# Performance work log

Hardware: AMD Instinct MI355X
Metric: run time of the kernel (lower is better)

Reference implementation:

```python
import jax, jax.numpy as jnp
import numpy as np

E = 2048      # embed_dim
H = 16        # num_heads
HD = E // H // 2   # differential head dim = 64
S = 2048      # seq len
B = 1         # batch
DEPTH = 12
LAMBDA_INIT = 0.8 - 0.6 * float(np.exp(-0.3 * DEPTH))
EPS = 1e-5


def setup_inputs() -> dict:
    key = jax.random.key(0)
    ks = jax.random.split(key, 12)
    n = lambda k, shape, s=1.0: (jax.random.normal(k, shape, dtype=jnp.float32) * s)
    return {
        "query": n(ks[0], (S, B, E)),
        "key": n(ks[1], (S, B, E)),
        "value": n(ks[2], (S, B, E)),
        "rel_pos": 0,
        "attn_mask": jnp.zeros((B, S), dtype=jnp.bool_),
        "Wq": n(ks[3], (E, E), 0.02),
        "Wk": n(ks[4], (E, E), 0.02),
        "Wv": n(ks[5], (E, E), 0.02),
        "Wo": n(ks[6], (E, E), 0.02),
        "lq1": n(ks[7], (HD,), 0.1),
        "lk1": n(ks[8], (HD,), 0.1),
        "lq2": n(ks[9], (HD,), 0.1),
        "lk2": n(ks[10], (HD,), 0.1),
        "subln_g": jnp.ones((2 * HD,), dtype=jnp.float32),
    }


def reference(query, key, value, rel_pos, attn_mask,
              Wq, Wk, Wv, Wo, lq1, lk1, lq2, lk2, subln_g):
    # (S,B,E) -> (B,S,E)
    q = jnp.einsum("sbe,fe->bsf", query, Wq)
    k = jnp.einsum("sbe,fe->bsf", key, Wk)
    v = jnp.einsum("sbe,fe->bsf", value, Wv)

    bsz, tgt_len, _ = q.shape
    scaling = HD ** -0.5

    q = q.reshape(bsz, tgt_len, 2 * H, HD).transpose(0, 2, 1, 3) * scaling  # (B,2H,S,hd)
    k = k.reshape(bsz, tgt_len, 2 * H, HD).transpose(0, 2, 1, 3)            # (B,2H,S,hd)
    v = v.reshape(bsz, tgt_len, H, 2 * HD).transpose(0, 2, 1, 3)            # (B,H,S,2hd)

    scores = jnp.einsum("bhqd,bhkd->bhqk", q, k)  # (B,2H,S,S)
    mask = jnp.where(attn_mask[:, None, None, :], -jnp.inf, 0.0).astype(scores.dtype)
    scores = jnp.nan_to_num(scores + mask)  # torch.nan_to_num: nan->0, -inf->finite min

    probs = jax.nn.softmax(scores.astype(jnp.float32), axis=-1).astype(scores.dtype)
    probs = jnp.clip(probs, -1e6, 1e6)  # clamp as in original (dropout is identity in eval)

    lam1 = jnp.exp(jnp.sum(lq1 * lk1))
    lam2 = jnp.exp(jnp.sum(lq2 * lk2))
    lam_full = lam1 - lam2 + LAMBDA_INIT

    probs = probs.reshape(bsz, H, 2, tgt_len, tgt_len)
    diff = probs[:, :, 0] - lam_full * probs[:, :, 1]   # (B,H,S,S)

    attn = jnp.einsum("bhqk,bhkd->bhqd", diff, v)       # (B,H,S,2hd)

    # RMSNorm over last dim with affine weight
    rms = jax.lax.rsqrt(jnp.mean(jnp.square(attn), axis=-1, keepdims=True) + EPS)
    attn = attn * rms * subln_g
    attn = attn * (1.0 - LAMBDA_INIT)

    attn = attn.transpose(0, 2, 1, 3).reshape(bsz, tgt_len, H * 2 * HD)  # (B,S,E)
    attn = attn.transpose(1, 0, 2)                                       # (S,B,E)
    return jnp.einsum("sbe,fe->sbf", attn, Wo)
```

## Files before the change

### kernel.cpp

```cpp
#include <hip/hip_runtime.h>
#include <stdint.h>

#define LAMBDA_INIT_F 0.7836057665f

typedef __bf16 bf16x8 __attribute__((ext_vector_type(8)));
typedef float  f32x4  __attribute__((ext_vector_type(4)));
typedef unsigned short u16x8 __attribute__((ext_vector_type(8)));
typedef unsigned short u16x4 __attribute__((ext_vector_type(4)));
typedef short s16x4 __attribute__((ext_vector_type(4)));

__device__ __forceinline__ unsigned short f2b(float f) {
    union { float f; unsigned u; } v; v.f = f;
    unsigned u = v.u;
    return (unsigned short)((u + 0x7fffu + ((u >> 16) & 1u)) >> 16);
}

__device__ __forceinline__ unsigned pk2(float a, float b) {
    unsigned ua = __float_as_uint(a) + 0x8000u;
    unsigned ub = __float_as_uint(b) + 0x8000u;
    return __builtin_amdgcn_perm(ub, ua, 0x07060302u);
}

#if __has_builtin(__builtin_amdgcn_exp2f)
#define EXP2(x) __builtin_amdgcn_exp2f(x)
#else
__device__ __forceinline__ float EXP2(float x) {
    float r; asm volatile("v_exp_f32 %0, %1\n\ts_nop 1" : "=v"(r) : "v"(x)); return r;
}
#endif

#define GLD16(gp, sp) __builtin_amdgcn_global_load_lds( \
    (const __attribute__((address_space(1))) void*)(uintptr_t)(gp), \
    (__attribute__((address_space(3))) void*)(uint32_t)(uintptr_t)(sp), 16, 0, 0)

__global__ __launch_bounds__(256) void cvt7(const float* __restrict__ s0, const float* __restrict__ s1,
                                            const float* __restrict__ s2, const float* __restrict__ s3,
                                            const float* __restrict__ s4, const float* __restrict__ s5,
                                            const float* __restrict__ s6,
                                            unsigned short* __restrict__ dst) {
    int z = blockIdx.y;
    const float* s = z == 0 ? s0 : z == 1 ? s1 : z == 2 ? s2 : z == 3 ? s3 : z == 4 ? s4 : z == 5 ? s5 : s6;
    unsigned short* d = dst + (size_t)z * 4194304;
    size_t i = ((size_t)blockIdx.x * 256 + threadIdx.x) * 8;
    float4 a = *(const float4*)(s + i);
    float4 b = *(const float4*)(s + i + 4);
    u16x8 o;
    o[0] = f2b(a.x); o[1] = f2b(a.y); o[2] = f2b(a.z); o[3] = f2b(a.w);
    o[4] = f2b(b.x); o[5] = f2b(b.y); o[6] = f2b(b.z); o[7] = f2b(b.w);
    *(u16x8*)(d + i) = o;
}

template <int OUT_BF16, int NT, int DO_VT, int WPB>
__global__ __launch_bounds__(256, WPB) void gemm_bt(const unsigned short* __restrict__ Abase,
                                                    const unsigned short* __restrict__ Bbase,
                                                    void* __restrict__ Cbase,
                                                    unsigned short* __restrict__ VT,
                                                    float alpha0) {
    constexpr int MI = (NT == 128) ? 4 : 2;
    __shared__ __align__(16) unsigned short As[128 * 32];
    __shared__ __align__(16) unsigned short Bs[NT * 32];
    const int tid = threadIdx.x;
    const int w = tid >> 6, lane = tid & 63;
    const int quad = lane >> 4, l16 = lane & 15;
    const int b = blockIdx.z;
    const unsigned short* A = Abase + (size_t)b * 4194304;
    const unsigned short* B = Bbase + (size_t)b * 4194304;
    const float alpha = (b == 0) ? alpha0 : 1.0f;
    const int m0 = blockIdx.y * 128, n0 = blockIdx.x * NT;
    const int wm = (NT == 128) ? (w >> 1) * 64 : w * 32;
    const int wn = (NT == 128) ? (w & 1) * 64 : 0;
    const int sr = lane >> 2;
    const int sc = (((lane & 3) ^ ((lane >> 3) & 3)) * 8);
    const int rsw = ((l16 >> 1) & 3);

    f32x4 zz = {0.f, 0.f, 0.f, 0.f};
    f32x4 acc[MI][4];
#pragma unroll
    for (int i = 0; i < MI; ++i)
#pragma unroll
        for (int jn = 0; jn < 4; ++jn) acc[i][jn] = zz;

    for (int k0 = 0; k0 < 2048; k0 += 32) {
        GLD16(A + (size_t)(m0 + w * 16 + sr) * 2048 + k0 + sc,      &As[(w * 16) * 32]);
        GLD16(A + (size_t)(m0 + 64 + w * 16 + sr) * 2048 + k0 + sc, &As[(64 + w * 16) * 32]);
        if (NT == 128) {
            GLD16(B + (size_t)(n0 + w * 16 + sr) * 2048 + k0 + sc,      &Bs[(w * 16) * 32]);
            GLD16(B + (size_t)(n0 + 64 + w * 16 + sr) * 2048 + k0 + sc, &Bs[(64 + (w * 16)) * 32]);
        } else {
            GLD16(B + (size_t)(n0 + w * 16 + sr) * 2048 + k0 + sc, &Bs[(w * 16) * 32]);
        }
        __syncthreads();
        bf16x8 af[MI], bfr[4];
#pragma unroll
        for (int i = 0; i < MI; ++i) af[i]  = *(const bf16x8*)&As[(wm + i * 16 + l16) * 32 + (quad ^ rsw) * 8];
#pragma unroll
        for (int i = 0; i < 4; ++i)  bfr[i] = *(const bf16x8*)&Bs[(wn + i * 16 + l16) * 32 + (quad ^ rsw) * 8];
#pragma unroll
        for (int i = 0; i < MI; ++i)
#pragma unroll
            for (int jn = 0; jn < 4; ++jn)
                acc[i][jn] = __builtin_amdgcn_mfma_f32_16x16x32_bf16(af[i], bfr[jn], acc[i][jn], 0, 0, 0);
        __syncthreads();
    }

    if (DO_VT && b == 2) {
#pragma unroll
        for (int i = 0; i < MI; ++i)
#pragma unroll
            for (int jn = 0; jn < 4; ++jn) {
                int n = n0 + wn + jn * 16 + l16;
                int m = m0 + wm + i * 16 + quad * 4;
                u16x4 o;
#pragma unroll
                for (int r = 0; r < 4; ++r) o[r] = f2b(acc[i][jn][r]);
                *(u16x4*)&VT[(size_t)n * 2048 + m] = o;
            }
    } else {
#pragma unroll
        for (int i = 0; i < MI; ++i)
#pragma unroll
            for (int jn = 0; jn < 4; ++jn)
#pragma unroll
                for (int r = 0; r < 4; ++r) {
                    int row = m0 + wm + i * 16 + quad * 4 + r;
                    int col = n0 + wn + jn * 16 + l16;
                    float v = acc[i][jn][r] * alpha;
                    if (OUT_BF16)
                        ((unsigned short*)Cbase + (size_t)b * 4194304)[(size_t)row * 2048 + col] = f2b(v);
                    else
                        ((float*)Cbase)[(size_t)row * 2048 + col] = v;
                }
    }
}

__global__ __launch_bounds__(256, 2) void diff_attn(const unsigned short* __restrict__ qb,
                                                    const unsigned short* __restrict__ kb,
                                                    const unsigned short* __restrict__ vt,
                                                    const float* __restrict__ lq1,
                                                    const float* __restrict__ lk1,
                                                    const float* __restrict__ lq2,
                                                    const float* __restrict__ lk2,
                                                    const float* __restrict__ g,
                                                    unsigned short* __restrict__ Aout) {
    __shared__ __align__(16) unsigned short Ks[128 * 128];
    __shared__ __align__(16) unsigned short Vs[128 * 128];
    __shared__ float lam_s;
    const int tid = threadIdx.x, w = tid >> 6, lane = tid & 63;
    const int quad = lane >> 4, l16 = lane & 15;
    const int j = blockIdx.y;
    const int q0 = blockIdx.x * 64;

    if (tid < 64) {
        float p1 = lq1[tid] * lk1[tid];
        float p2 = lq2[tid] * lk2[tid];
        for (int off = 32; off; off >>= 1) { p1 += __shfl_xor(p1, off, 64); p2 += __shfl_xor(p2, off, 64); }
        if (tid == 0) lam_s = __expf(p1) - __expf(p2) + LAMBDA_INIT_F;
    }

    bf16x8 qf[2][2];
#pragma unroll
    for (int p = 0; p < 2; ++p)
#pragma unroll
        for (int dh = 0; dh < 2; ++dh)
            qf[p][dh] = *(const bf16x8*)&qb[(size_t)(q0 + w * 16 + l16) * 2048 + j * 128 + p * 64 + dh * 32 + quad * 8];

    f32x4 O[2][8];
#pragma unroll
    for (int p = 0; p < 2; ++p)
#pragma unroll
        for (int i = 0; i < 8; ++i)
#pragma unroll
            for (int r = 0; r < 4; ++r) O[p][i][r] = 0.f;
    float lsum[2] = {0.f, 0.f};

    const int srow = lane >> 4;

    for (int kv0 = 0; kv0 < 2048; kv0 += 128) {
#pragma unroll
        for (int t = 0; t < 8; ++t) {
            int rb = (w * 8 + t) * 4;
            int row = rb + srow;
            int cbs = (((lane & 15) ^ (row & 15)) * 8);
            GLD16(kb + (size_t)(kv0 + row) * 2048 + j * 128 + cbs, &Ks[rb * 128]);
            GLD16(vt + (size_t)(j * 128 + row) * 2048 + kv0 + cbs, &Vs[rb * 128]);
        }
        __syncthreads();

        s16x4 pf[2][8];
#pragma unroll
        for (int p = 0; p < 2; ++p) {
#pragma unroll
            for (int i = 0; i < 8; ++i) {
                bf16x8 a0 = *(const bf16x8*)&Ks[(i * 16 + l16) * 128 + ((p * 8 + quad) ^ l16) * 8];
                bf16x8 a1 = *(const bf16x8*)&Ks[(i * 16 + l16) * 128 + ((p * 8 + 4 + quad) ^ l16) * 8];
                f32x4 s = {0.f, 0.f, 0.f, 0.f};
                s = __builtin_amdgcn_mfma_f32_16x16x32_bf16(a0, qf[p][0], s, 0, 0, 0);
                s = __builtin_amdgcn_mfma_f32_16x16x32_bf16(a1, qf[p][1], s, 0, 0, 0);
                float e0 = EXP2(s[0]), e1 = EXP2(s[1]), e2 = EXP2(s[2]), e3 = EXP2(s[3]);
                lsum[p] += (e0 + e1) + (e2 + e3);
                unsigned d0 = pk2(e0, e1), d1 = pk2(e2, e3);
                s16x4 pv;
                pv[0] = (short)(d0 & 0xffff); pv[1] = (short)(d0 >> 16);
                pv[2] = (short)(d1 & 0xffff); pv[3] = (short)(d1 >> 16);
                pf[p][i] = pv;
            }
        }
#pragma unroll
        for (int i = 0; i < 8; ++i) {
#pragma unroll
            for (int dt = 0; dt < 8; ++dt) {
                int blk = (i * 2 + (quad >> 1)) ^ l16;
                s16x4 vf = *(const s16x4*)&Vs[(dt * 16 + l16) * 128 + blk * 8 + (quad & 1) * 4];
                O[0][dt] = __builtin_amdgcn_mfma_f32_16x16x16bf16_1k(vf, pf[0][i], O[0][dt], 0, 0, 0);
                O[1][dt] = __builtin_amdgcn_mfma_f32_16x16x16bf16_1k(vf, pf[1][i], O[1][dt], 0, 0, 0);
            }
        }
        __syncthreads();
    }

#pragma unroll
    for (int p = 0; p < 2; ++p) {
        lsum[p] += __shfl_xor(lsum[p], 16, 64);
        lsum[p] += __shfl_xor(lsum[p], 32, 64);
    }
    const float inv1 = 1.0f / lsum[0];
    const float inv2 = lam_s / lsum[1];

    float ssum = 0.f;
#pragma unroll
    for (int dt = 0; dt < 8; ++dt)
#pragma unroll
        for (int r = 0; r < 4; ++r) {
            float v = O[0][dt][r] * inv1 - O[1][dt][r] * inv2;
            O[0][dt][r] = v;
            ssum += v * v;
        }
    ssum += __shfl_xor(ssum, 16, 64);
    ssum += __shfl_xor(ssum, 32, 64);
    const float rms = rsqrtf(ssum * (1.0f / 128.0f) + 1e-5f) * (1.0f - LAMBDA_INIT_F);

#pragma unroll
    for (int dt = 0; dt < 8; ++dt) {
        float4 g4 = *(const float4*)&g[dt * 16 + quad * 4];
        u16x4 o;
        o[0] = f2b(O[0][dt][0] * rms * g4.x);
        o[1] = f2b(O[0][dt][1] * rms * g4.y);
        o[2] = f2b(O[0][dt][2] * rms * g4.z);
        o[3] = f2b(O[0][dt][3] * rms * g4.w);
        *(u16x4*)&Aout[(size_t)(q0 + w * 16 + l16) * 2048 + j * 128 + dt * 16 + quad * 4] = o;
    }
}

extern "C" void kernel_launch(void* const* d_in, const int* in_sizes, int n_in,
                              void* d_out, int out_size, void* d_ws, size_t ws_size,
                              hipStream_t stream) {
    const float* query = (const float*)d_in[0];
    const float* key   = (const float*)d_in[1];
    const float* value = (const float*)d_in[2];
    const float* Wq  = (const float*)d_in[5];
    const float* Wk  = (const float*)d_in[6];
    const float* Wv  = (const float*)d_in[7];
    const float* Wo  = (const float*)d_in[8];
    const float* lq1 = (const float*)d_in[9];
    const float* lk1 = (const float*)d_in[10];
    const float* lq2 = (const float*)d_in[11];
    const float* lk2 = (const float*)d_in[12];
    const float* g   = (const float*)d_in[13];

    char* ws = (char*)d_ws;
    const size_t MB = 1ull << 20;
    const size_t N4 = 4194304;
    unsigned short* qb  = (unsigned short*)(ws + 0 * MB);
    unsigned short* vt  = (unsigned short*)(ws + 16 * MB);
    unsigned short* Aat = (unsigned short*)(ws + 24 * MB);
    unsigned short* Xq  = (unsigned short*)(ws + 32 * MB);
    float* lamp = (float*)(ws + 96 * MB);
    (void)lamp;

    const float alpha_q = 0.125f * 1.44269504f;

    cvt7<<<dim3(2048, 7), dim3(256), 0, stream>>>(query, key, value, Wq, Wk, Wv, Wo, Xq);
    gemm_bt<1, 128, 1, 3><<<dim3(16, 16, 3), dim3(256), 0, stream>>>(Xq, Xq + 3 * N4, (void*)qb, vt, alpha_q);
    diff_attn<<<dim3(32, 16), dim3(256), 0, stream>>>(qb, qb + N4, vt, lq1, lk1, lq2, lk2, g, Aat);
    gemm_bt<0, 64, 0, 2><<<dim3(32, 16, 1), dim3(256), 0, stream>>>(Aat, Xq + 6 * N4, d_out, nullptr, 1.0f);
}
```

Baseline: 334.6 us.

## Halve attention KV tile, raise occupancy, truncate bf16 packing, widen output GEMM tile

The attention kernel now streams K/V in 64-row tiles instead of 128, which halves LDS use and sets launch bounds to 4 blocks per CU. The V swizzle is adjusted to match the narrower 64-column rows. The probability packing switches from round-to-nearest to plain truncation, saving two adds per pair at some loss of precision. The QKV GEMM's launch bound drops from 3 to 2 blocks per CU, and the output GEMM moves from a 64-wide to a 128-wide N tile with half the blocks.

```diff
diff --git a/kernel.cpp b/kernel.cpp
--- a/kernel.cpp
+++ b/kernel.cpp
@@ -15,10 +15,8 @@
     return (unsigned short)((u + 0x7fffu + ((u >> 16) & 1u)) >> 16);
 }
 
-__device__ __forceinline__ unsigned pk2(float a, float b) {
-    unsigned ua = __float_as_uint(a) + 0x8000u;
-    unsigned ub = __float_as_uint(b) + 0x8000u;
-    return __builtin_amdgcn_perm(ub, ua, 0x07060302u);
+__device__ __forceinline__ unsigned pk2t(float a, float b) {
+    return __builtin_amdgcn_perm(__float_as_uint(b), __float_as_uint(a), 0x07060302u);
 }
 
 #if __has_builtin(__builtin_amdgcn_exp2f)
@@ -50,12 +48,12 @@
     *(u16x8*)(d + i) = o;
 }
 
-template <int OUT_BF16, int NT, int DO_VT, int WPB>
-__global__ __launch_bounds__(256, WPB) void gemm_bt(const unsigned short* __restrict__ Abase,
-                                                    const unsigned short* __restrict__ Bbase,
-                                                    void* __restrict__ Cbase,
-                                                    unsigned short* __restrict__ VT,
-                                                    float alpha0) {
+template <int OUT_BF16, int NT, int DO_VT>
+__global__ __launch_bounds__(256, 2) void gemm_bt(const unsigned short* __restrict__ Abase,
+                                                  const unsigned short* __restrict__ Bbase,
+                                                  void* __restrict__ Cbase,
+                                                  unsigned short* __restrict__ VT,
+                                                  float alpha0) {
     constexpr int MI = (NT == 128) ? 4 : 2;
     __shared__ __align__(16) unsigned short As[128 * 32];
     __shared__ __align__(16) unsigned short Bs[NT * 32];
@@ -133,7 +131,7 @@
     }
 }
 
-__global__ __launch_bounds__(256, 2) void diff_attn(const unsigned short* __restrict__ qb,
+__global__ __launch_bounds__(256, 4) void diff_attn(const unsigned short* __restrict__ qb,
                                                     const unsigned short* __restrict__ kb,
                                                     const unsigned short* __restrict__ vt,
                                                     const float* __restrict__ lq1,
@@ -142,8 +140,8 @@
                                                     const float* __restrict__ lk2,
                                                     const float* __restrict__ g,
                                                     unsigned short* __restrict__ Aout) {
-    __shared__ __align__(16) unsigned short Ks[128 * 128];
-    __shared__ __align__(16) unsigned short Vs[128 * 128];
+    __shared__ __align__(16) unsigned short Ks[64 * 128];
+    __shared__ __align__(16) unsigned short Vs[128 * 64];
     __shared__ float lam_s;
     const int tid = threadIdx.x, w = tid >> 6, lane = tid & 63;
     const int quad = lane >> 4, l16 = lane & 15;
@@ -173,24 +171,28 @@
             for (int r = 0; r < 4; ++r) O[p][i][r] = 0.f;
     float lsum[2] = {0.f, 0.f};
 
-    const int srow = lane >> 4;
-
-    for (int kv0 = 0; kv0 < 2048; kv0 += 128) {
-#pragma unroll
-        for (int t = 0; t < 8; ++t) {
-            int rb = (w * 8 + t) * 4;
-            int row = rb + srow;
-            int cbs = (((lane & 15) ^ (row & 15)) * 8);
-            GLD16(kb + (size_t)(kv0 + row) * 2048 + j * 128 + cbs, &Ks[rb * 128]);
-            GLD16(vt + (size_t)(j * 128 + row) * 2048 + kv0 + cbs, &Vs[rb * 128]);
-        }
-        __syncthreads();
-
-        s16x4 pf[2][8];
+    const int ksrow = lane >> 4;
+    const int vsrow = lane >> 3;
+
+    for (int kv0 = 0; kv0 < 2048; kv0 += 64) {
+#pragma unroll
+        for (int t = 0; t < 4; ++t) {
+            int krb = (w * 4 + t) * 4;
+            int krow = krb + ksrow;
+            int kcb = (((lane & 15) ^ (krow & 15)) * 8);
+            GLD16(kb + (size_t)(kv0 + krow) * 2048 + j * 128 + kcb, &Ks[krb * 128]);
+            int vrb = (w * 4 + t) * 8;
+            int vrow = vrb + vsrow;
+            int vcb = (((lane & 7) ^ (vrow & 7)) * 8);
+            GLD16(vt + (size_t)(j * 128 + vrow) * 2048 + kv0 + vcb, &Vs[vrb * 64]);
+        }
+        __syncthreads();
+
+        s16x4 pf[2][4];
 #pragma unroll
         for (int p = 0; p < 2; ++p) {
 #pragma unroll
-            for (int i = 0; i < 8; ++i) {
+            for (int i = 0; i < 4; ++i) {
                 bf16x8 a0 = *(const bf16x8*)&Ks[(i * 16 + l16) * 128 + ((p * 8 + quad) ^ l16) * 8];
                 bf16x8 a1 = *(const bf16x8*)&Ks[(i * 16 + l16) * 128 + ((p * 8 + 4 + quad) ^ l16) * 8];
                 f32x4 s = {0.f, 0.f, 0.f, 0.f};
@@ -198,7 +200,7 @@
                 s = __builtin_amdgcn_mfma_f32_16x16x32_bf16(a1, qf[p][1], s, 0, 0, 0);
                 float e0 = EXP2(s[0]), e1 = EXP2(s[1]), e2 = EXP2(s[2]), e3 = EXP2(s[3]);
                 lsum[p] += (e0 + e1) + (e2 + e3);
-                unsigned d0 = pk2(e0, e1), d1 = pk2(e2, e3);
+                unsigned d0 = pk2t(e0, e1), d1 = pk2t(e2, e3);
                 s16x4 pv;
                 pv[0] = (short)(d0 & 0xffff); pv[1] = (short)(d0 >> 16);
                 pv[2] = (short)(d1 & 0xffff); pv[3] = (short)(d1 >> 16);
@@ -206,11 +208,12 @@
             }
         }
 #pragma unroll
-        for (int i = 0; i < 8; ++i) {
+        for (int i = 0; i < 4; ++i) {
 #pragma unroll
             for (int dt = 0; dt < 8; ++dt) {
-                int blk = (i * 2 + (quad >> 1)) ^ l16;
-                s16x4 vf = *(const s16x4*)&Vs[(dt * 16 + l16) * 128 + blk * 8 + (quad & 1) * 4];
+                int row = dt * 16 + l16;
+                int blk = (i * 2 + (quad >> 1)) ^ (row & 7);
+                s16x4 vf = *(const s16x4*)&Vs[row * 64 + blk * 8 + (quad & 1) * 4];
                 O[0][dt] = __builtin_amdgcn_mfma_f32_16x16x16bf16_1k(vf, pf[0][i], O[0][dt], 0, 0, 0);
                 O[1][dt] = __builtin_amdgcn_mfma_f32_16x16x16bf16_1k(vf, pf[1][i], O[1][dt], 0, 0, 0);
             }
@@ -274,13 +277,11 @@
     unsigned short* vt  = (unsigned short*)(ws + 16 * MB);
     unsigned short* Aat = (unsigned short*)(ws + 24 * MB);
     unsigned short* Xq  = (unsigned short*)(ws + 32 * MB);
-    float* lamp = (float*)(ws + 96 * MB);
-    (void)lamp;
 
     const float alpha_q = 0.125f * 1.44269504f;
 
     cvt7<<<dim3(2048, 7), dim3(256), 0, stream>>>(query, key, value, Wq, Wk, Wv, Wo, Xq);
-    gemm_bt<1, 128, 1, 3><<<dim3(16, 16, 3), dim3(256), 0, stream>>>(Xq, Xq + 3 * N4, (void*)qb, vt, alpha_q);
+    gemm_bt<1, 128, 1><<<dim3(16, 16, 3), dim3(256), 0, stream>>>(Xq, Xq + 3 * N4, (void*)qb, vt, alpha_q);
     diff_attn<<<dim3(32, 16), dim3(256), 0, stream>>>(qb, qb + N4, vt, lq1, lk1, lq2, lk2, g, Aat);
-    gemm_bt<0, 64, 0, 2><<<dim3(32, 16, 1), dim3(256), 0, stream>>>(Aat, Xq + 6 * N4, d_out, nullptr, 1.0f);
-}
+    gemm_bt<0, 128, 0><<<dim3(16, 16, 1), dim3(256), 0, stream>>>(Aat, Xq + 6 * N4, d_out, nullptr, 1.0f);
+}
```

Result: slower. 406.7 us (+21.5%).
